# Optimization experiments

Hardware: AMD Instinct MI355X
Metric: run time of the kernel (lower is better)

Reference implementation:

```python
import jax, jax.numpy as jnp
import numpy as np

B_GRAPHS = 64      # number of graphs in the batch
NODES_PER_G = 1600 # nodes per graph (equal-size for simplicity; math is ragged-safe via segment_sum)
N = B_GRAPHS * NODES_PER_G  # 102400 nodes
F_DIM = 128
K_CLUSTERS = 16
AVG_DEG = 32
E = N * AVG_DEG  # 3276800 edges


def setup_inputs() -> dict:
    key = jax.random.key(0)
    k1, k2, k3, k4, k5, k6 = jax.random.split(key, 6)
    x = jax.random.normal(k1, (N, F_DIM), jnp.float32)
    W = jax.random.normal(k2, (F_DIM, K_CLUSTERS), jnp.float32) * (1.0 / np.sqrt(F_DIM))
    b = jnp.zeros((K_CLUSTERS,), jnp.float32)
    # edges are constrained to lie within a graph (adjacency is block-diagonal across graphs)
    g = jax.random.randint(k3, (E,), 0, B_GRAPHS)
    edge_src = jax.random.randint(k4, (E,), 0, NODES_PER_G) + g * NODES_PER_G
    edge_dst = jax.random.randint(k5, (E,), 0, NODES_PER_G) + g * NODES_PER_G
    edge_weight = jax.random.uniform(k6, (E,), jnp.float32)
    batch = jnp.repeat(jnp.arange(B_GRAPHS), NODES_PER_G)  # sorted graph ids, as batch2ptr requires
    return {"x": x, "W": W, "b": b, "edge_weight": edge_weight,
            "edge_src": edge_src, "edge_dst": edge_dst, "batch": batch}


def reference(x, W, b, edge_weight, edge_src, edge_dst, batch):
    K = W.shape[1]
    Bn = B_GRAPHS
    n_nodes = x.shape[0]
    # forward() applies softmax once, then mincut_pool applies softmax again (temp=1.0)
    s = jax.nn.softmax(x @ W + b, axis=-1)
    s = jax.nn.softmax(s, axis=-1)                      # [N, K]
    # d = adj.sum(axis=0): column sums of the sparse adjacency
    deg = jax.ops.segment_sum(edge_weight, edge_dst, num_segments=n_nodes)  # [N]
    # M = A @ S without materializing block-diagonal C_bd:  M[i] = sum_j w_ij * s[j]
    M = jax.ops.segment_sum(edge_weight[:, None] * s[edge_dst], edge_src, num_segments=n_nodes)  # [N, K]
    # out_adj blocks: S_b^T A_b S_b  -> [B, K, K]  (C_bd^T A C_bd is block-diagonal)
    out_adj = jax.ops.segment_sum(s[:, :, None] * M[:, None, :], batch, num_segments=Bn)
    # mincut loss = -trace(C^T A C) / trace(C^T D C)
    mincut_num = jnp.sum(jnp.trace(out_adj, axis1=1, axis2=2))
    mincut_den = jnp.sum(deg * jnp.sum(s * s, axis=1))
    mincut_loss = -mincut_num / mincut_den
    # CC blocks: S_b^T S_b -> [B, K, K]
    CC = jax.ops.segment_sum(s[:, :, None] * s[:, None, :], batch, num_segments=Bn)
    cc_norm = jnp.sqrt(jnp.sum(CC * CC, axis=(1, 2)))   # per-graph Frobenius norm of CC block
    eye_div_k = jnp.eye(K, dtype=x.dtype) / jnp.sqrt(jnp.asarray(K, x.dtype))
    diff = CC / cc_norm[:, None, None] - eye_div_k
    ortho_loss = jnp.mean(jnp.sqrt(jnp.sum(diff * diff, axis=(1, 2))))
    # mask diagonal of pooled adjacency, then symmetric degree-normalize
    out_adj = out_adj * (1.0 - jnp.eye(K, dtype=x.dtype))
    d_pool = jnp.sqrt(jnp.sum(out_adj, axis=2)) + 1e-12  # [B, K] row sums -> sqrt + eps
    out_adj_n = out_adj / (d_pool[:, :, None] * d_pool[:, None, :])
    # out_x: per-graph S_b^T X_b, vstacked -> [B*K, F]; module applies SELU
    out_x = jax.ops.segment_sum(s[:, :, None] * x[:, None, :], batch, num_segments=Bn)
    out_x = jax.nn.selu(out_x.reshape(Bn * K, -1))
    return out_x, out_adj_n, mincut_loss, ortho_loss
```

## Files before the change

### kernel.cpp

```cpp
#include <hip/hip_runtime.h>
#include <math.h>

#define NN 102400
#define FD 128
#define KC 16
#define BG 64
#define NPG 1600
#define NE 3276800
#define HB 512
#define EH (NE / HB)
#define EPT (EH / 256)
#define BINS 256
#define RPB 400
#define NPB 200

__device__ __forceinline__ void glob_addf(float* p, float v) {
  unsafeAtomicAdd(p, v);
}
__device__ __forceinline__ unsigned f2bf(float f) {
  unsigned u = __float_as_uint(f);
  u += 0x7FFFu + ((u >> 16) & 1u);
  return (u >> 16) & 0xFFFFu;
}
__device__ __forceinline__ float bf2f(unsigned h) {
  return __uint_as_float(h << 16);
}

__global__ __launch_bounds__(256, 4) void k_s2(const float* __restrict__ x,
    const float* __restrict__ W, const float* __restrict__ bb,
    const int* __restrict__ esrc, float* __restrict__ s,
    unsigned* __restrict__ blkhist, float* __restrict__ cc_part,
    float* __restrict__ outx_part) {
  __shared__ float st[NPB * KC];
  __shared__ unsigned h[BINS];
  const int t = threadIdx.x, b = blockIdx.x;
  const int g = b >> 3, sub = b & 7;
  const int n0 = g * NPG + sub * NPB;
  h[t] = 0u;
  __syncthreads();
  const int e0 = b * EH;
  for (int i = t; i < EH; i += 256) {
    unsigned bin = (unsigned)esrc[e0 + i] / (unsigned)RPB;
    atomicAdd(&h[bin], 1u);
  }
  __syncthreads();
  blkhist[t * HB + b] = h[t];
  if (t < NPB) {
    float acc[KC];
#pragma unroll
    for (int k = 0; k < KC; ++k) acc[k] = bb[k];
    const float4* xr = (const float4*)(x + (size_t)(n0 + t) * FD);
#pragma unroll 4
    for (int c = 0; c < FD / 4; ++c) {
      float4 v = xr[c];
      const float* wr = W + c * 4 * KC;
#pragma unroll
      for (int k = 0; k < KC; ++k)
        acc[k] += v.x * wr[k] + v.y * wr[KC + k] + v.z * wr[2 * KC + k] + v.w * wr[3 * KC + k];
    }
#pragma unroll
    for (int r = 0; r < 2; ++r) {
      float m = acc[0];
#pragma unroll
      for (int k = 1; k < KC; ++k) m = fmaxf(m, acc[k]);
      float sum = 0.f;
#pragma unroll
      for (int k = 0; k < KC; ++k) { acc[k] = expf(acc[k] - m); sum += acc[k]; }
      float inv = 1.f / sum;
#pragma unroll
      for (int k = 0; k < KC; ++k) acc[k] *= inv;
    }
#pragma unroll
    for (int k = 0; k < KC; ++k) st[t * KC + k] = acc[k];
    float4* so = (float4*)(s + (size_t)(n0 + t) * KC);
    so[0] = make_float4(acc[0], acc[1], acc[2], acc[3]);
    so[1] = make_float4(acc[4], acc[5], acc[6], acc[7]);
    so[2] = make_float4(acc[8], acc[9], acc[10], acc[11]);
    so[3] = make_float4(acc[12], acc[13], acc[14], acc[15]);
  }
  __syncthreads();
  const int j = t & 127, h2 = t >> 7;
  const int kc = t >> 4, lc = t & 15;
  float accX[8] = {0.f, 0.f, 0.f, 0.f, 0.f, 0.f, 0.f, 0.f};
  float accC = 0.f;
  for (int i = 0; i < NPB; ++i) {
    const float xv = x[(size_t)(n0 + i) * FD + j];
    const float* si = st + i * KC;
#pragma unroll
    for (int kk = 0; kk < 8; ++kk) accX[kk] = fmaf(si[h2 * 8 + kk], xv, accX[kk]);
    accC = fmaf(si[kc], si[lc], accC);
  }
#pragma unroll
  for (int kk = 0; kk < 8; ++kk)
    outx_part[(size_t)b * 2048 + (h2 * 8 + kk) * 128 + j] = accX[kk];
  cc_part[b * 256 + t] = accC;
}

__global__ __launch_bounds__(512) void k_scan_a(unsigned* __restrict__ blkhist,
    unsigned* __restrict__ gtot, unsigned* __restrict__ azero) {
  __shared__ unsigned wsum[8];
  const int t = threadIdx.x, bin = blockIdx.x;
  const int lane = t & 63;
  const unsigned zi = (unsigned)bin * 512u + (unsigned)t;
  if (zi < 16400u) azero[zi] = 0u;
  unsigned v = blkhist[bin * HB + t];
  unsigned inc = v;
#pragma unroll
  for (int o = 1; o < 64; o <<= 1) {
    unsigned nb = __shfl_up(inc, o, 64);
    if (lane >= o) inc += nb;
  }
  if (lane == 63) wsum[t >> 6] = inc;
  __syncthreads();
  if (t == 0) {
    unsigned run = 0;
#pragma unroll
    for (int i = 0; i < 8; ++i) { unsigned c = wsum[i]; wsum[i] = run; run += c; }
    gtot[bin] = run;
  }
  __syncthreads();
  blkhist[bin * HB + t] = inc - v + wsum[t >> 6];
}

__global__ __launch_bounds__(64) void k_scan_b(const unsigned* __restrict__ gtot,
    unsigned* __restrict__ gbase) {
  const int t = threadIdx.x;
  unsigned v0 = gtot[t * 4], v1 = gtot[t * 4 + 1];
  unsigned v2 = gtot[t * 4 + 2], v3 = gtot[t * 4 + 3];
  unsigned sum = v0 + v1 + v2 + v3;
  unsigned inc = sum;
#pragma unroll
  for (int o = 1; o < 64; o <<= 1) {
    unsigned nb = __shfl_up(inc, o, 64);
    if (t >= o) inc += nb;
  }
  unsigned ex = inc - sum;
  gbase[t * 4] = ex;
  gbase[t * 4 + 1] = ex + v0;
  gbase[t * 4 + 2] = ex + v0 + v1;
  gbase[t * 4 + 3] = ex + v0 + v1 + v2;
  if (t == 63) gbase[BINS] = inc;
}

__global__ __launch_bounds__(256, 2) void k_scatter2(const float* __restrict__ ew,
    const int* __restrict__ esrc, const int* __restrict__ edst,
    const unsigned* __restrict__ blkhist, const unsigned* __restrict__ gbase,
    unsigned short* __restrict__ skey, unsigned* __restrict__ pay) {
  __shared__ unsigned cur[BINS];
  __shared__ unsigned gadj[BINS];
  __shared__ unsigned wsum[4];
  __shared__ unsigned pays[EH];
  __shared__ unsigned gofs[EH];
  __shared__ unsigned short keys[EH];
  const int t = threadIdx.x, b = blockIdx.x;
  cur[t] = 0u;
  const unsigned gstart = gbase[t] + blkhist[t * HB + b];
  __syncthreads();
  unsigned rpay[EPT], rmeta[EPT];
  const int e0 = b * EH;
#pragma unroll
  for (int i = 0; i < EPT; ++i) {
    const int e = e0 + t + i * 256;
    int s0 = esrc[e], d0 = edst[e];
    float w = ew[e];
    unsigned bin = (unsigned)s0 / (unsigned)RPB;
    unsigned g = bin >> 2;
    rmeta[i] = (bin << 16) | ((unsigned)s0 - bin * RPB);
    rpay[i] = (((unsigned)d0 - g * NPG) << 16) | f2bf(w);
    atomicAdd(&cur[bin], 1u);
  }
  __syncthreads();
  {
    unsigned v = cur[t];
    unsigned inc = v;
#pragma unroll
    for (int o = 1; o < 64; o <<= 1) {
      unsigned nb = __shfl_up(inc, o, 64);
      if ((t & 63) >= o) inc += nb;
    }
    if ((t & 63) == 63) wsum[t >> 6] = inc;
    __syncthreads();
    if (t == 0) {
      unsigned run = 0;
#pragma unroll
      for (int i = 0; i < 4; ++i) { unsigned c = wsum[i]; wsum[i] = run; run += c; }
    }
    __syncthreads();
    const unsigned boff = inc - v + wsum[t >> 6];
    cur[t] = boff;
    gadj[t] = gstart - boff;
  }
  __syncthreads();
#pragma unroll
  for (int i = 0; i < EPT; ++i) {
    const unsigned bin = rmeta[i] >> 16;
    const unsigned pos = atomicAdd(&cur[bin], 1u);
    pays[pos] = rpay[i];
    keys[pos] = (unsigned short)(rmeta[i] & 0xFFFFu);
    gofs[pos] = gadj[bin] + pos;
  }
  __syncthreads();
  for (int p = t; p < EH; p += 256) {
    const unsigned ga = gofs[p];
    pay[ga] = pays[p];
    skey[ga] = keys[p];
  }
}

__global__ __launch_bounds__(1024, 1) void k_msc3(const float* __restrict__ s,
    const unsigned short* __restrict__ skey, const unsigned* __restrict__ pay,
    const unsigned* __restrict__ gbase, float* __restrict__ adj_raw,
    float* __restrict__ den) {
  __shared__ float SL[NPG * 17];
  __shared__ unsigned Ml[RPB * 17];
  __shared__ float P[1024];
  __shared__ float scr[16];
  const int t = threadIdx.x;
  const int bin = (blockIdx.x & 7) * 32 + (blockIdx.x >> 3);
  const int g = bin >> 2;
  const int q = bin & 3;
  const float4* sg4 = (const float4*)(s + (size_t)g * NPG * KC);
  for (int u4 = t; u4 < NPG * KC / 4; u4 += 1024) {
    float4 v = sg4[u4];
    const int u = u4 * 4;
    float* d = &SL[(u >> 4) * 17 + (u & 15)];
    d[0] = v.x; d[1] = v.y; d[2] = v.z; d[3] = v.w;
  }
  for (int i = t; i < RPB * 17; i += 1024) Ml[i] = 0u;
  __syncthreads();
  const unsigned gb = gbase[bin], ge = gbase[bin + 1];
  const int l = t & 15;
  const int gid = t >> 4;
  const float FXS = 16777216.f;
  float dacc = 0.f;
  unsigned e = gb + gid;
  for (; e + 192 < ge; e += 256) {
    unsigned pk0 = pay[e],       pk1 = pay[e + 64];
    unsigned pk2 = pay[e + 128], pk3 = pay[e + 192];
    unsigned sk0 = skey[e],       sk1 = skey[e + 64];
    unsigned sk2 = skey[e + 128], sk3 = skey[e + 192];
    float sv0 = SL[(pk0 >> 16) * 17 + l];
    float sv1 = SL[(pk1 >> 16) * 17 + l];
    float sv2 = SL[(pk2 >> 16) * 17 + l];
    float sv3 = SL[(pk3 >> 16) * 17 + l];
    float t0 = bf2f(pk0 & 0xFFFFu) * sv0;
    float t1 = bf2f(pk1 & 0xFFFFu) * sv1;
    float t2 = bf2f(pk2 & 0xFFFFu) * sv2;
    float t3 = bf2f(pk3 & 0xFFFFu) * sv3;
    dacc = fmaf(t0, sv0, dacc);
    dacc = fmaf(t1, sv1, dacc);
    dacc = fmaf(t2, sv2, dacc);
    dacc = fmaf(t3, sv3, dacc);
    atomicAdd(&Ml[sk0 * 17 + l], __float2uint_rn(t0 * FXS));
    atomicAdd(&Ml[sk1 * 17 + l], __float2uint_rn(t1 * FXS));
    atomicAdd(&Ml[sk2 * 17 + l], __float2uint_rn(t2 * FXS));
    atomicAdd(&Ml[sk3 * 17 + l], __float2uint_rn(t3 * FXS));
  }
  for (; e < ge; e += 64) {
    unsigned pk0 = pay[e];
    unsigned sk0 = skey[e];
    float sv0 = SL[(pk0 >> 16) * 17 + l];
    float t0 = bf2f(pk0 & 0xFFFFu) * sv0;
    dacc = fmaf(t0, sv0, dacc);
    atomicAdd(&Ml[sk0 * 17 + l], __float2uint_rn(t0 * FXS));
  }
  __syncthreads();
  const int ck = (t >> 4) & 15, cl = t & 15, sub = t >> 8;
  float pacc = 0.f;
  const float* SLq = SL + q * RPB * 17;
#pragma unroll 4
  for (int ii = 0; ii < RPB / 4; ++ii) {
    const int r = sub + 4 * ii;
    pacc = fmaf(SLq[r * 17 + ck], (float)Ml[r * 17 + cl], pacc);
  }
  P[t] = pacc;
#pragma unroll
  for (int o = 32; o > 0; o >>= 1) dacc += __shfl_down(dacc, o, 64);
  if ((t & 63) == 0) scr[t >> 6] = dacc;
  __syncthreads();
  if (t < 256) glob_addf(adj_raw + g * 256 + t,
                         (P[t] + P[t + 256] + P[t + 512] + P[t + 768])
                             * 5.9604644775390625e-8f);
  if (t == 0) {
    float sum = 0.f;
#pragma unroll
    for (int i = 0; i < 16; ++i) sum += scr[i];
    glob_addf(den, sum);
  }
}

__device__ __forceinline__ float bred(float v, float* scr) {
#pragma unroll
  for (int o = 32; o > 0; o >>= 1) v += __shfl_down(v, o, 64);
  __syncthreads();
  if ((threadIdx.x & 63) == 0) scr[threadIdx.x >> 6] = v;
  __syncthreads();
  return scr[0] + scr[1] + scr[2] + scr[3];
}

__global__ __launch_bounds__(256) void k_post(const float* __restrict__ adj_raw,
    const float* __restrict__ cc_part, const float* __restrict__ outx_part,
    float* __restrict__ out, float* __restrict__ scal, unsigned* __restrict__ done) {
  const int b = blockIdx.x, t = threadIdx.x;
  const int k = t >> 4, l = t & 15;
  __shared__ float m[16 * 17];
  __shared__ float dk[16];
  __shared__ float scr[4];
  const float raw = adj_raw[b * 256 + t];
  const float masked = (k == l) ? 0.f : raw;
  m[k * 17 + l] = masked;
  __syncthreads();
  if (t < 16) {
    float rs = 0.f;
#pragma unroll
    for (int ll = 0; ll < 16; ++ll) rs += m[t * 17 + ll];
    dk[t] = sqrtf(rs) + 1e-12f;
  }
  __syncthreads();
  out[131072 + b * 256 + t] = masked / (dk[k] * dk[l]);
  float tr = bred((k == l) ? raw : 0.f, scr);
  if (t == 0) glob_addf(scal + 1, tr);
  float c = 0.f;
#pragma unroll
  for (int u = 0; u < 8; ++u) c += cc_part[(b * 8 + u) * 256 + t];
  float n2 = bred(c * c, scr);
  float diff = c / sqrtf(n2) - ((k == l) ? 0.25f : 0.f);
  float d2 = bred(diff * diff, scr);
  if (t == 0) glob_addf(scal + 2, sqrtf(d2));
  for (int idx = b * 256 + t; idx < 131072; idx += 16384) {
    const int gg = idx >> 11, v = idx & 2047;
    float xv = 0.f;
#pragma unroll
    for (int u = 0; u < 8; ++u) xv += outx_part[(size_t)(gg * 8 + u) * 2048 + v];
    out[idx] = xv > 0.f ? 1.0507009873554805f * xv
                        : 1.0507009873554805f * 1.6732632423543772f * expm1f(xv);
  }
  __syncthreads();
  if (t == 0) {
    __threadfence();
    unsigned v = __hip_atomic_fetch_add(done, 1u, __ATOMIC_ACQ_REL,
                                        __HIP_MEMORY_SCOPE_AGENT);
    if (v == 63u) {
      float den   = __hip_atomic_load(scal + 0, __ATOMIC_RELAXED, __HIP_MEMORY_SCOPE_AGENT);
      float num   = __hip_atomic_load(scal + 1, __ATOMIC_RELAXED, __HIP_MEMORY_SCOPE_AGENT);
      float ortho = __hip_atomic_load(scal + 2, __ATOMIC_RELAXED, __HIP_MEMORY_SCOPE_AGENT);
      out[147456] = -num / den;
      out[147457] = ortho * (1.f / 64.f);
    }
  }
}

extern "C" void kernel_launch(void* const* d_in, const int* in_sizes, int n_in,
                              void* d_out, int out_size, void* d_ws, size_t ws_size,
                              hipStream_t stream) {
  const float* x  = (const float*)d_in[0];
  const float* W  = (const float*)d_in[1];
  const float* bb = (const float*)d_in[2];
  const float* ew = (const float*)d_in[3];
  const int* esrc = (const int*)d_in[4];
  const int* edst = (const int*)d_in[5];
  float* out = (float*)d_out;
  float* ws = (float*)d_ws;

  float* s_buf    = ws;
  float* adj_raw  = s_buf + (size_t)NN * KC;
  float* scal     = adj_raw + 16384;
  unsigned* done  = (unsigned*)(scal + 8);
  float* cc_part  = (float*)(done + 8);
  float* outx_part= cc_part + 131072;
  unsigned* gtot  = (unsigned*)(outx_part + 1048576);
  unsigned* gbase = gtot + BINS;
  unsigned* blkhist = gbase + 264;
  unsigned short* skey = (unsigned short*)(blkhist + (size_t)BINS * HB);
  unsigned* pay = (unsigned*)(skey + NE);

  k_s2<<<HB, 256, 0, stream>>>(x, W, bb, esrc, s_buf, blkhist, cc_part, outx_part);
  k_scan_a<<<BINS, 512, 0, stream>>>(blkhist, gtot, (unsigned*)adj_raw);
  k_scan_b<<<1, 64, 0, stream>>>(gtot, gbase);
  k_scatter2<<<HB, 256, 0, stream>>>(ew, esrc, edst, blkhist, gbase, skey, pay);
  k_msc3<<<BINS, 1024, 0, stream>>>(s_buf, skey, pay, gbase, adj_raw, scal);
  k_post<<<64, 256, 0, stream>>>(adj_raw, cc_part, outx_part, out, scal, done);
}
```

Before: 218.0 us.

## Rebalance block partitioning, drop scan kernel, shrink scatter LDS, move CC to post

Several changes at once. The edge/node partition grows from 512 to 640 blocks of 160 nodes, and the block histogram is stored as 16-bit. The separate global-scan kernel is removed: its prefix over bin totals is recomputed inside the scatter and msc kernels. The scatter kernel replaces the per-edge global offset array with a byte bin map, which cuts LDS use and allows higher occupancy. The msc edge loop is unrolled from 4 to 8 loads, and the S^T S (CC) computation moves from the softmax kernel into the post kernel, which rereads s per graph. This saves a launch and some LDS but makes the 64-block post kernel do more serial work.

```diff
diff --git a/kernel.cpp b/kernel.cpp
--- a/kernel.cpp
+++ b/kernel.cpp
@@ -7,12 +7,12 @@
 #define BG 64
 #define NPG 1600
 #define NE 3276800
-#define HB 512
+#define HB 640
 #define EH (NE / HB)
 #define EPT (EH / 256)
 #define BINS 256
 #define RPB 400
-#define NPB 200
+#define NPB 160
 
 __device__ __forceinline__ void glob_addf(float* p, float v) {
   unsafeAtomicAdd(p, v);
@@ -29,12 +29,11 @@
 __global__ __launch_bounds__(256, 4) void k_s2(const float* __restrict__ x,
     const float* __restrict__ W, const float* __restrict__ bb,
     const int* __restrict__ esrc, float* __restrict__ s,
-    unsigned* __restrict__ blkhist, float* __restrict__ cc_part,
-    float* __restrict__ outx_part) {
+    unsigned short* __restrict__ blkhist, float* __restrict__ outx_part) {
   __shared__ float st[NPB * KC];
   __shared__ unsigned h[BINS];
   const int t = threadIdx.x, b = blockIdx.x;
-  const int g = b >> 3, sub = b & 7;
+  const int g = b / 10, sub = b % 10;
   const int n0 = g * NPG + sub * NPB;
   h[t] = 0u;
   __syncthreads();
@@ -44,7 +43,7 @@
     atomicAdd(&h[bin], 1u);
   }
   __syncthreads();
-  blkhist[t * HB + b] = h[t];
+  blkhist[t * HB + b] = (unsigned short)h[t];
   if (t < NPB) {
     float acc[KC];
 #pragma unroll
@@ -80,28 +79,24 @@
   }
   __syncthreads();
   const int j = t & 127, h2 = t >> 7;
-  const int kc = t >> 4, lc = t & 15;
   float accX[8] = {0.f, 0.f, 0.f, 0.f, 0.f, 0.f, 0.f, 0.f};
-  float accC = 0.f;
   for (int i = 0; i < NPB; ++i) {
     const float xv = x[(size_t)(n0 + i) * FD + j];
     const float* si = st + i * KC;
 #pragma unroll
     for (int kk = 0; kk < 8; ++kk) accX[kk] = fmaf(si[h2 * 8 + kk], xv, accX[kk]);
-    accC = fmaf(si[kc], si[lc], accC);
   }
 #pragma unroll
   for (int kk = 0; kk < 8; ++kk)
     outx_part[(size_t)b * 2048 + (h2 * 8 + kk) * 128 + j] = accX[kk];
-  cc_part[b * 256 + t] = accC;
-}
-
-__global__ __launch_bounds__(512) void k_scan_a(unsigned* __restrict__ blkhist,
+}
+
+__global__ __launch_bounds__(640) void k_scan_a(unsigned short* __restrict__ blkhist,
     unsigned* __restrict__ gtot, unsigned* __restrict__ azero) {
-  __shared__ unsigned wsum[8];
+  __shared__ unsigned wsum[10];
   const int t = threadIdx.x, bin = blockIdx.x;
   const int lane = t & 63;
-  const unsigned zi = (unsigned)bin * 512u + (unsigned)t;
+  const unsigned zi = (unsigned)bin * 640u + (unsigned)t;
   if (zi < 16400u) azero[zi] = 0u;
   unsigned v = blkhist[bin * HB + t];
   unsigned inc = v;
@@ -115,46 +110,41 @@
   if (t == 0) {
     unsigned run = 0;
 #pragma unroll
-    for (int i = 0; i < 8; ++i) { unsigned c = wsum[i]; wsum[i] = run; run += c; }
+    for (int i = 0; i < 10; ++i) { unsigned c = wsum[i]; wsum[i] = run; run += c; }
     gtot[bin] = run;
   }
   __syncthreads();
-  blkhist[bin * HB + t] = inc - v + wsum[t >> 6];
-}
-
-__global__ __launch_bounds__(64) void k_scan_b(const unsigned* __restrict__ gtot,
-    unsigned* __restrict__ gbase) {
-  const int t = threadIdx.x;
-  unsigned v0 = gtot[t * 4], v1 = gtot[t * 4 + 1];
-  unsigned v2 = gtot[t * 4 + 2], v3 = gtot[t * 4 + 3];
-  unsigned sum = v0 + v1 + v2 + v3;
-  unsigned inc = sum;
-#pragma unroll
-  for (int o = 1; o < 64; o <<= 1) {
-    unsigned nb = __shfl_up(inc, o, 64);
-    if (t >= o) inc += nb;
-  }
-  unsigned ex = inc - sum;
-  gbase[t * 4] = ex;
-  gbase[t * 4 + 1] = ex + v0;
-  gbase[t * 4 + 2] = ex + v0 + v1;
-  gbase[t * 4 + 3] = ex + v0 + v1 + v2;
-  if (t == 63) gbase[BINS] = inc;
-}
-
-__global__ __launch_bounds__(256, 2) void k_scatter2(const float* __restrict__ ew,
+  blkhist[bin * HB + t] = (unsigned short)(inc - v + wsum[t >> 6]);
+}
+
+__global__ __launch_bounds__(256, 4) void k_scatter2(const float* __restrict__ ew,
     const int* __restrict__ esrc, const int* __restrict__ edst,
-    const unsigned* __restrict__ blkhist, const unsigned* __restrict__ gbase,
+    const unsigned short* __restrict__ blkhist, const unsigned* __restrict__ gtot,
     unsigned short* __restrict__ skey, unsigned* __restrict__ pay) {
   __shared__ unsigned cur[BINS];
   __shared__ unsigned gadj[BINS];
   __shared__ unsigned wsum[4];
   __shared__ unsigned pays[EH];
-  __shared__ unsigned gofs[EH];
   __shared__ unsigned short keys[EH];
+  __shared__ unsigned char bmap[EH];
   const int t = threadIdx.x, b = blockIdx.x;
+  const unsigned gv = gtot[t];
+  unsigned ginc = gv;
+#pragma unroll
+  for (int o = 1; o < 64; o <<= 1) {
+    unsigned nb = __shfl_up(ginc, o, 64);
+    if ((t & 63) >= o) ginc += nb;
+  }
+  if ((t & 63) == 63) wsum[t >> 6] = ginc;
+  __syncthreads();
+  if (t == 0) {
+    unsigned run = 0;
+#pragma unroll
+    for (int i = 0; i < 4; ++i) { unsigned c = wsum[i]; wsum[i] = run; run += c; }
+  }
+  __syncthreads();
+  const unsigned gstart = (ginc - gv + wsum[t >> 6]) + blkhist[t * HB + b];
   cur[t] = 0u;
-  const unsigned gstart = gbase[t] + blkhist[t * HB + b];
   __syncthreads();
   unsigned rpay[EPT], rmeta[EPT];
   const int e0 = b * EH;
@@ -197,11 +187,12 @@
     const unsigned pos = atomicAdd(&cur[bin], 1u);
     pays[pos] = rpay[i];
     keys[pos] = (unsigned short)(rmeta[i] & 0xFFFFu);
-    gofs[pos] = gadj[bin] + pos;
+    bmap[pos] = (unsigned char)bin;
   }
   __syncthreads();
   for (int p = t; p < EH; p += 256) {
-    const unsigned ga = gofs[p];
+    const unsigned bin = bmap[p];
+    const unsigned ga = gadj[bin] + p;
     pay[ga] = pays[p];
     skey[ga] = keys[p];
   }
@@ -209,16 +200,34 @@
 
 __global__ __launch_bounds__(1024, 1) void k_msc3(const float* __restrict__ s,
     const unsigned short* __restrict__ skey, const unsigned* __restrict__ pay,
-    const unsigned* __restrict__ gbase, float* __restrict__ adj_raw,
+    const unsigned* __restrict__ gtot, float* __restrict__ adj_raw,
     float* __restrict__ den) {
   __shared__ float SL[NPG * 17];
   __shared__ unsigned Ml[RPB * 17];
   __shared__ float P[1024];
   __shared__ float scr[16];
+  __shared__ unsigned gbl[257];
   const int t = threadIdx.x;
   const int bin = (blockIdx.x & 7) * 32 + (blockIdx.x >> 3);
   const int g = bin >> 2;
   const int q = bin & 3;
+  if (t < 64) {
+    unsigned v0 = gtot[t * 4], v1 = gtot[t * 4 + 1];
+    unsigned v2 = gtot[t * 4 + 2], v3 = gtot[t * 4 + 3];
+    unsigned sum = v0 + v1 + v2 + v3;
+    unsigned inc = sum;
+#pragma unroll
+    for (int o = 1; o < 64; o <<= 1) {
+      unsigned nb = __shfl_up(inc, o, 64);
+      if (t >= o) inc += nb;
+    }
+    unsigned ex = inc - sum;
+    gbl[t * 4] = ex;
+    gbl[t * 4 + 1] = ex + v0;
+    gbl[t * 4 + 2] = ex + v0 + v1;
+    gbl[t * 4 + 3] = ex + v0 + v1 + v2;
+    if (t == 63) gbl[256] = inc;
+  }
   const float4* sg4 = (const float4*)(s + (size_t)g * NPG * KC);
   for (int u4 = t; u4 < NPG * KC / 4; u4 += 1024) {
     float4 v = sg4[u4];
@@ -228,33 +237,53 @@
   }
   for (int i = t; i < RPB * 17; i += 1024) Ml[i] = 0u;
   __syncthreads();
-  const unsigned gb = gbase[bin], ge = gbase[bin + 1];
+  const unsigned gb = gbl[bin], ge = gbl[bin + 1];
   const int l = t & 15;
   const int gid = t >> 4;
   const float FXS = 16777216.f;
   float dacc = 0.f;
   unsigned e = gb + gid;
-  for (; e + 192 < ge; e += 256) {
+  for (; e + 448 < ge; e += 512) {
     unsigned pk0 = pay[e],       pk1 = pay[e + 64];
     unsigned pk2 = pay[e + 128], pk3 = pay[e + 192];
+    unsigned pk4 = pay[e + 256], pk5 = pay[e + 320];
+    unsigned pk6 = pay[e + 384], pk7 = pay[e + 448];
     unsigned sk0 = skey[e],       sk1 = skey[e + 64];
     unsigned sk2 = skey[e + 128], sk3 = skey[e + 192];
+    unsigned sk4 = skey[e + 256], sk5 = skey[e + 320];
+    unsigned sk6 = skey[e + 384], sk7 = skey[e + 448];
     float sv0 = SL[(pk0 >> 16) * 17 + l];
     float sv1 = SL[(pk1 >> 16) * 17 + l];
     float sv2 = SL[(pk2 >> 16) * 17 + l];
     float sv3 = SL[(pk3 >> 16) * 17 + l];
+    float sv4 = SL[(pk4 >> 16) * 17 + l];
+    float sv5 = SL[(pk5 >> 16) * 17 + l];
+    float sv6 = SL[(pk6 >> 16) * 17 + l];
+    float sv7 = SL[(pk7 >> 16) * 17 + l];
     float t0 = bf2f(pk0 & 0xFFFFu) * sv0;
     float t1 = bf2f(pk1 & 0xFFFFu) * sv1;
     float t2 = bf2f(pk2 & 0xFFFFu) * sv2;
     float t3 = bf2f(pk3 & 0xFFFFu) * sv3;
+    float t4 = bf2f(pk4 & 0xFFFFu) * sv4;
+    float t5 = bf2f(pk5 & 0xFFFFu) * sv5;
+    float t6 = bf2f(pk6 & 0xFFFFu) * sv6;
+    float t7 = bf2f(pk7 & 0xFFFFu) * sv7;
     dacc = fmaf(t0, sv0, dacc);
     dacc = fmaf(t1, sv1, dacc);
     dacc = fmaf(t2, sv2, dacc);
     dacc = fmaf(t3, sv3, dacc);
+    dacc = fmaf(t4, sv4, dacc);
+    dacc = fmaf(t5, sv5, dacc);
+    dacc = fmaf(t6, sv6, dacc);
+    dacc = fmaf(t7, sv7, dacc);
     atomicAdd(&Ml[sk0 * 17 + l], __float2uint_rn(t0 * FXS));
     atomicAdd(&Ml[sk1 * 17 + l], __float2uint_rn(t1 * FXS));
     atomicAdd(&Ml[sk2 * 17 + l], __float2uint_rn(t2 * FXS));
     atomicAdd(&Ml[sk3 * 17 + l], __float2uint_rn(t3 * FXS));
+    atomicAdd(&Ml[sk4 * 17 + l], __float2uint_rn(t4 * FXS));
+    atomicAdd(&Ml[sk5 * 17 + l], __float2uint_rn(t5 * FXS));
+    atomicAdd(&Ml[sk6 * 17 + l], __float2uint_rn(t6 * FXS));
+    atomicAdd(&Ml[sk7 * 17 + l], __float2uint_rn(t7 * FXS));
   }
   for (; e < ge; e += 64) {
     unsigned pk0 = pay[e];
@@ -299,13 +328,14 @@
 }
 
 __global__ __launch_bounds__(256) void k_post(const float* __restrict__ adj_raw,
-    const float* __restrict__ cc_part, const float* __restrict__ outx_part,
+    const float* __restrict__ s, const float* __restrict__ outx_part,
     float* __restrict__ out, float* __restrict__ scal, unsigned* __restrict__ done) {
   const int b = blockIdx.x, t = threadIdx.x;
   const int k = t >> 4, l = t & 15;
   __shared__ float m[16 * 17];
   __shared__ float dk[16];
   __shared__ float scr[4];
+  __shared__ float st2[100 * KC];
   const float raw = adj_raw[b * 256 + t];
   const float masked = (k == l) ? 0.f : raw;
   m[k * 17 + l] = masked;
@@ -320,9 +350,15 @@
   out[131072 + b * 256 + t] = masked / (dk[k] * dk[l]);
   float tr = bred((k == l) ? raw : 0.f, scr);
   if (t == 0) glob_addf(scal + 1, tr);
+  const float* sG = s + (size_t)b * NPG * KC;
   float c = 0.f;
-#pragma unroll
-  for (int u = 0; u < 8; ++u) c += cc_part[(b * 8 + u) * 256 + t];
+  for (int ch = 0; ch < 16; ++ch) {
+    __syncthreads();
+    for (int u = t; u < 100 * KC; u += 256) st2[u] = sG[ch * 100 * KC + u];
+    __syncthreads();
+#pragma unroll 4
+    for (int i = 0; i < 100; ++i) c = fmaf(st2[i * KC + k], st2[i * KC + l], c);
+  }
   float n2 = bred(c * c, scr);
   float diff = c / sqrtf(n2) - ((k == l) ? 0.25f : 0.f);
   float d2 = bred(diff * diff, scr);
@@ -331,7 +367,7 @@
     const int gg = idx >> 11, v = idx & 2047;
     float xv = 0.f;
 #pragma unroll
-    for (int u = 0; u < 8; ++u) xv += outx_part[(size_t)(gg * 8 + u) * 2048 + v];
+    for (int u = 0; u < 10; ++u) xv += outx_part[(size_t)(gg * 10 + u) * 2048 + v];
     out[idx] = xv > 0.f ? 1.0507009873554805f * xv
                         : 1.0507009873554805f * 1.6732632423543772f * expm1f(xv);
   }
@@ -366,18 +402,15 @@
   float* adj_raw  = s_buf + (size_t)NN * KC;
   float* scal     = adj_raw + 16384;
   unsigned* done  = (unsigned*)(scal + 8);
-  float* cc_part  = (float*)(done + 8);
-  float* outx_part= cc_part + 131072;
-  unsigned* gtot  = (unsigned*)(outx_part + 1048576);
-  unsigned* gbase = gtot + BINS;
-  unsigned* blkhist = gbase + 264;
-  unsigned short* skey = (unsigned short*)(blkhist + (size_t)BINS * HB);
+  float* outx_part= (float*)(done + 8);
+  unsigned* gtot  = (unsigned*)(outx_part + (size_t)HB * 2048);
+  unsigned short* blkhist = (unsigned short*)(gtot + BINS);
+  unsigned short* skey = blkhist + (size_t)BINS * HB;
   unsigned* pay = (unsigned*)(skey + NE);
 
-  k_s2<<<HB, 256, 0, stream>>>(x, W, bb, esrc, s_buf, blkhist, cc_part, outx_part);
-  k_scan_a<<<BINS, 512, 0, stream>>>(blkhist, gtot, (unsigned*)adj_raw);
-  k_scan_b<<<1, 64, 0, stream>>>(gtot, gbase);
-  k_scatter2<<<HB, 256, 0, stream>>>(ew, esrc, edst, blkhist, gbase, skey, pay);
-  k_msc3<<<BINS, 1024, 0, stream>>>(s_buf, skey, pay, gbase, adj_raw, scal);
-  k_post<<<64, 256, 0, stream>>>(adj_raw, cc_part, outx_part, out, scal, done);
-}
+  k_s2<<<HB, 256, 0, stream>>>(x, W, bb, esrc, s_buf, blkhist, outx_part);
+  k_scan_a<<<BINS, 640, 0, stream>>>(blkhist, gtot, (unsigned*)adj_raw);
+  k_scatter2<<<HB, 256, 0, stream>>>(ew, esrc, edst, blkhist, gtot, skey, pay);
+  k_msc3<<<BINS, 1024, 0, stream>>>(s_buf, skey, pay, gtot, adj_raw, scal);
+  k_post<<<64, 256, 0, stream>>>(adj_raw, s_buf, outx_part, out, scal, done);
+}
```

Result: slower. 259.6 us (+19.1%).
